# Kernel optimization log

Hardware: AMD Instinct MI355X
Metric: run time of the kernel (lower is better)

The kernel has to match this reference:

```python
import jax, jax.numpy as jnp
import numpy as np
from jax import lax

B, C, H, W = 1, 128, 56, 56
NH, NG, KS = 4, 1, 3
CG = C // NG          # channels per group
CH = C // NH          # channels per head
NHG = NH // NG        # heads per group
SCALE = CH ** -0.5


def _norm_grid(h, w, n):
    # matches _get_normalized_grid: (y, x) order, each normalized to [-1, 1]
    y = jnp.arange(h, dtype=jnp.float32) / (h - 1.0) * 2.0 - 1.0
    x = jnp.arange(w, dtype=jnp.float32) / (w - 1.0) * 2.0 - 1.0
    g = jnp.stack(jnp.meshgrid(y, x, indexing='ij'), axis=-1)  # (h, w, 2)
    return jnp.broadcast_to(g[None], (n, h, w, 2))


def _grid_sample(img, grid):
    # F.grid_sample: bilinear, align_corners=True, zeros padding; grid is (x, y) in [-1, 1]
    n, c, hi, wi = img.shape
    gs = grid.shape[1:-1]
    gx = grid[..., 0].reshape(n, -1)
    gy = grid[..., 1].reshape(n, -1)
    fx = (gx + 1.0) * 0.5 * (wi - 1)
    fy = (gy + 1.0) * 0.5 * (hi - 1)
    x0 = jnp.floor(fx)
    y0 = jnp.floor(fy)
    wx = fx - x0
    wy = fy - y0
    x0 = x0.astype(jnp.int32)
    y0 = y0.astype(jnp.int32)
    imgf = img.reshape(n, c, hi * wi)

    def corner(xi, yi, wgt):
        valid = (xi >= 0) & (xi < wi) & (yi >= 0) & (yi < hi)
        idx = jnp.clip(yi, 0, hi - 1) * wi + jnp.clip(xi, 0, wi - 1)
        vals = jax.vmap(lambda im, ii: jnp.take(im, ii, axis=1))(imgf, idx)  # (n, c, P)
        return vals * (wgt * valid)[:, None, :]

    out = (corner(x0, y0, (1 - wx) * (1 - wy)) + corner(x0 + 1, y0, wx * (1 - wy))
           + corner(x0, y0 + 1, (1 - wx) * wy) + corner(x0 + 1, y0 + 1, wx * wy))
    return out.reshape((n, c) + gs)


def _conv1x1(t, w, b):
    return jnp.einsum('bchw,oc->bohw', t, w) + b[None, :, None, None]


def _forward(x, query, dw_w, dw_b, ln_w, ln_b, pw_w, k_w, k_b, v_w, v_b, out_w, out_b, rpe_table):
    # conv_offset: depthwise 3x3 (stride 1, pad 1) -> channel LayerNorm -> GELU -> 1x1 to 2ch (no bias)
    qg = query.reshape(B * NG, CG, H, W)
    t = lax.conv_general_dilated(qg, dw_w, (1, 1), ((1, 1), (1, 1)),
                                 dimension_numbers=('NCHW', 'OIHW', 'NCHW'),
                                 feature_group_count=CG) + dw_b[None, :, None, None]
    mu = t.mean(axis=1, keepdims=True)
    var = ((t - mu) ** 2).mean(axis=1, keepdims=True)
    t = (t - mu) / jnp.sqrt(var + 1e-5) * ln_w[None, :, None, None] + ln_b[None, :, None, None]
    t = jax.nn.gelu(t, approximate=False)
    offset = jnp.einsum('bchw,oc->bohw', t, pw_w)  # (BG, 2, Hk, Wk) in (y, x) order
    Hk, Wk = offset.shape[-2:]
    n_sample = Hk * Wk

    # tanh-scaled offsets (scale_offset_range=True, factor 0.5)
    rng = jnp.array([1.0 / (Hk - 1.0), 1.0 / (Wk - 1.0)], jnp.float32).reshape(1, 2, 1, 1)
    offset = jnp.tanh(offset) * rng * 0.5
    offset = jnp.transpose(offset, (0, 2, 3, 1))  # (BG, Hk, Wk, 2)

    ref = _norm_grid(Hk, Wk, B * NG)
    rwo = offset + ref  # no clamp in the scale_offset_range branch

    # sample K/V features at deformed locations
    xs = _grid_sample(x.reshape(B * NG, CG, H, W), rwo[..., ::-1])  # (BG, CG, Hk, Wk)
    xs = xs.reshape(B, C, 1, n_sample)

    q = query.reshape(B * NH, CH, H * W)
    k = _conv1x1(xs, k_w, k_b).reshape(B * NH, CH, n_sample)
    v = _conv1x1(xs, v_w, v_b).reshape(B * NH, CH, n_sample)

    attn = jnp.einsum('bcm,bcn->bmn', q, k) * SCALE  # (B*NH, HW, n_sample)

    # relative position bias via bilinear lookup of rpe_table at displacements
    rpe = jnp.broadcast_to(rpe_table[None], (B,) + rpe_table.shape).reshape(B * NG, NHG, 2 * H - 1, 2 * W - 1)
    qgrid = _norm_grid(H, W, B * NG)
    disp = (qgrid.reshape(B * NG, H * W, 2)[:, :, None, :]
            - rwo.reshape(B * NG, n_sample, 2)[:, None, :, :]) * 0.5  # (BG, HW, n_sample, 2)
    bias = _grid_sample(rpe, disp[..., ::-1]).reshape(B * NH, H * W, n_sample)

    attn = jax.nn.softmax(attn + bias, axis=2)
    out = jnp.einsum('bmn,bcn->bcm', attn, v).reshape(B, C, H, W)
    return _conv1x1(out, out_w, out_b)


def setup_inputs() -> dict:
    key = jax.random.key(0)
    ks = jax.random.split(key, 8)
    f = lambda k, sh, s=0.02: jax.random.normal(k, sh, jnp.float32) * s
    return {
        'x': jax.random.normal(ks[0], (B, C, H, W), jnp.float32),
        'query': jax.random.normal(ks[1], (B, C, H, W), jnp.float32),
        'dw_w': f(ks[2], (CG, 1, KS, KS)),
        'dw_b': jnp.zeros((CG,), jnp.float32),
        'ln_w': jnp.ones((CG,), jnp.float32),
        'ln_b': jnp.zeros((CG,), jnp.float32),
        'pw_w': f(ks[3], (2, CG)),
        'k_w': f(ks[4], (C, C)),
        'k_b': jnp.zeros((C,), jnp.float32),
        'v_w': f(ks[5], (C, C)),
        'v_b': jnp.zeros((C,), jnp.float32),
        'out_w': f(ks[6], (C, C)),
        'out_b': jnp.zeros((C,), jnp.float32),
        'rpe_table': f(ks[7], (NH, 2 * H - 1, 2 * W - 1), 0.01),
    }


def reference(x, query, dw_w, dw_b, ln_w, ln_b, pw_w, k_w, k_b, v_w, v_b, out_w, out_b, rpe_table):
    return _forward(x, query, dw_w, dw_b, ln_w, ln_b, pw_w, k_w, k_b, v_w, v_b, out_w, out_b, rpe_table)
```

## Files before the change

kernel.cpp:

```cpp
#include <hip/hip_runtime.h>
#include <hip/hip_bf16.h>
#include <math.h>

#define HH 56
#define WW 56
#define HW 3136
#define NHEAD 4
#define RP 111
#define TP 113
#define TPE 12769
#define SCALE 0.17677669529663687f
#define LOG2E 1.44269504088896f
#define QSC (SCALE * LOG2E)
#define GHW 12544
#define NCHUNK 14
#define CLEN 224
#define BLEN 448
#define NSTEP 7

typedef unsigned short ushortT;
typedef __attribute__((ext_vector_type(8))) short short8v;
typedef __attribute__((ext_vector_type(16))) float f32x16;

#define OFF_RWO  0u
#define OFF_AA   8192u
#define OFF_W4   12288u
#define OFF_KBF  24832u
#define OFF_VBF  225536u
#define OFF_QBF  426240u
#define OFF_KWT  1028352u
#define OFF_VWT  1044736u
#define OFF_OWT  1061120u
#define OFF_XT   1077504u
#define OFF_QT   1478912u
#define OFF_TP2  1880320u
#define OFF_ATT2 1982976u
#define OFF_SUM  2384384u

__device__ __forceinline__ ushortT f2bf(float f) {
    unsigned u = __float_as_uint(f);
    u += 0x7fffu + ((u >> 16) & 1u);
    return (ushortT)(u >> 16);
}

__device__ __forceinline__ unsigned cvtpk(float lo, float hi) {
    unsigned r;
    asm("v_cvt_pk_bf16_f32 %0, %1, %2" : "=v"(r) : "v"(lo), "v"(hi));
    return r;
}

__device__ __forceinline__ float fexp2(float x) {
    float r;
    asm("v_exp_f32 %0, %1" : "=v"(r) : "v"(x));
    return r;
}

__global__ __launch_bounds__(256) void prep_all_kernel(
    const float* __restrict__ kw, const float* __restrict__ vw, const float* __restrict__ ow,
    const float* __restrict__ rpe, const float* __restrict__ x, const float* __restrict__ query,
    float* __restrict__ kwT, float* __restrict__ vwT, float* __restrict__ owT,
    float2* __restrict__ tp2, float* __restrict__ xT, float* __restrict__ qT,
    ushortT* __restrict__ qbf) {
    const int job = blockIdx.y;
    __shared__ float tile[32][33];
    if (job < 3) {
        int i = blockIdx.x * 256 + threadIdx.x;
        if (i >= 16384) return;
        const float* srcw = (job == 0) ? kw : (job == 1) ? vw : ow;
        float* dstw       = (job == 0) ? kwT : (job == 1) ? vwT : owT;
        dstw[(i & 127) * 128 + (i >> 7)] = srcw[i];
    } else if (job == 3) {
        int i = blockIdx.x * 256 + threadIdx.x;
        if (i >= NHEAD * TPE) return;
        int hd = i / TPE, r = i % TPE;
        int py = r / TP, px = r % TP;
        float v0 = 0.f, v1 = 0.f;
        if (py >= 1 && py <= RP) {
            if (px >= 1 && px <= RP) v0 = rpe[hd * RP * RP + (py - 1) * RP + (px - 1)] * LOG2E;
            if (px <= RP - 1)        v1 = rpe[hd * RP * RP + (py - 1) * RP + px] * LOG2E;
        }
        tp2[i] = make_float2(v0, v1);
    } else {
        int bx = blockIdx.x;
        if (bx >= 392) return;
        const float* src = (job == 5) ? query : x;
        float* dst       = (job == 5) ? qT : xT;
        int pt = (bx % 98) * 32, ct = (bx / 98) * 32;
        int jj = threadIdx.x & 31, ii = threadIdx.x >> 5;
#pragma unroll
        for (int r = 0; r < 4; r++)
            tile[ii + r * 8][jj] = src[(ct + ii + r * 8) * HW + pt + jj];
        __syncthreads();
#pragma unroll
        for (int r = 0; r < 4; r++) {
            int p = pt + ii + r * 8, cc = ct + jj;
            float val = tile[jj][ii + r * 8];
            dst[p * 128 + cc] = val;
            if (job == 5)
                qbf[(size_t)((cc >> 5) * HW + p) * 32 + (cc & 31)] = f2bf(val * QSC);
        }
    }
}

__device__ __forceinline__ float wave_sum(float v) {
#pragma unroll
    for (int o = 1; o < 64; o <<= 1) v += __shfl_xor(v, o);
    return v;
}

__global__ __launch_bounds__(128) void offset_kernel(
    const float* __restrict__ qT, const float* __restrict__ dww, const float* __restrict__ dwb,
    const float* __restrict__ lnw, const float* __restrict__ lnb, const float* __restrict__ pww,
    float* __restrict__ rwo, int* __restrict__ aa, float* __restrict__ w4) {
    int p = blockIdx.x;
    int c = threadIdx.x;
    int h = p / WW, w = p % WW;

    float t = dwb[c];
#pragma unroll
    for (int ky = 0; ky < 3; ky++) {
        int yy = h + ky - 1;
        if ((unsigned)yy < (unsigned)HH) {
#pragma unroll
            for (int kx = 0; kx < 3; kx++) {
                int xx = w + kx - 1;
                if ((unsigned)xx < (unsigned)WW)
                    t += qT[(yy * WW + xx) * 128 + c] * dww[c * 9 + ky * 3 + kx];
            }
        }
    }

    __shared__ float sred[4];
    int wid = c >> 6, lane0 = ((c & 63) == 0);

    float s = wave_sum(t);
    if (lane0) sred[wid] = s;
    __syncthreads();
    float mu = (sred[0] + sred[1]) * (1.f / 128.f);
    float d = t - mu;
    __syncthreads();
    s = wave_sum(d * d);
    if (lane0) sred[wid] = s;
    __syncthreads();
    float var = (sred[0] + sred[1]) * (1.f / 128.f);

    float tn = d / sqrtf(var + 1e-5f) * lnw[c] + lnb[c];
    float g = 0.5f * tn * (1.f + erff(tn * 0.70710678118654752f));

    float sy = wave_sum(g * pww[c]);
    float sx = wave_sum(g * pww[128 + c]);
    __syncthreads();
    if (lane0) { sred[wid] = sy; sred[2 + wid] = sx; }
    __syncthreads();
    if (c == 0) {
        float thy = tanhf(sred[0] + sred[1]);
        float thx = tanhf(sred[2] + sred[3]);
        rwo[p * 2]     = thy * (0.5f / 55.f) + ((float)h * (2.f / 55.f) - 1.f);
        rwo[p * 2 + 1] = thx * (0.5f / 55.f) + ((float)w * (2.f / 55.f) - 1.f);
        float ty = 55.f - (float)h - 0.25f * thy;
        float tx = 55.f - (float)w - 0.25f * thx;
        float tyf = floorf(ty), txf = floorf(tx);
        float wy = ty - tyf, wx = tx - txf;
        aa[p] = ((int)tyf) * TP + (int)txf + TP + 1;
        float4 wv;
        wv.x = (1.f - wx) * (1.f - wy);
        wv.y = wx * (1.f - wy);
        wv.z = (1.f - wx) * wy;
        wv.w = wx * wy;
        ((float4*)w4)[p] = wv;
    }
}

__global__ __launch_bounds__(128) void sample_kv_kernel(
    const float* __restrict__ xT, const float* __restrict__ rwo,
    const float* __restrict__ kwT, const float* __restrict__ vwT,
    const float* __restrict__ kb, const float* __restrict__ vb,
    ushortT* __restrict__ kbf, ushortT* __restrict__ vbf) {
    int n0 = blockIdx.x * 8;
    int tid = threadIdx.x;

    __shared__ float xs[128 * 9];
    __shared__ int   cidx[8][4];
    __shared__ float cw[8][4];
    __shared__ ushortT kst[8][128];

    if (tid < 8) {
        int n = n0 + tid;
        float gy = rwo[2 * n], gx = rwo[2 * n + 1];
        float fx = (gx + 1.f) * 27.5f;
        float fy = (gy + 1.f) * 27.5f;
        float x0f = floorf(fx), y0f = floorf(fy);
        float wx = fx - x0f, wy = fy - y0f;
        int x0 = (int)x0f, y0 = (int)y0f;
#pragma unroll
        for (int k = 0; k < 4; k++) {
            int xi = x0 + (k & 1), yi = y0 + (k >> 1);
            float wgt = ((k & 1) ? wx : 1.f - wx) * ((k >> 1) ? wy : 1.f - wy);
            bool v = (xi >= 0) && (xi < WW) && (yi >= 0) && (yi < HH);
            cidx[tid][k] = min(max(yi, 0), HH - 1) * WW + min(max(xi, 0), WW - 1);
            cw[tid][k] = v ? wgt : 0.f;
        }
    }
    __syncthreads();

#pragma unroll
    for (int j = 0; j < 8; j++) {
        float s = cw[j][0] * xT[cidx[j][0] * 128 + tid]
                + cw[j][1] * xT[cidx[j][1] * 128 + tid]
                + cw[j][2] * xT[cidx[j][2] * 128 + tid]
                + cw[j][3] * xT[cidx[j][3] * 128 + tid];
        xs[tid * 9 + j] = s;
    }
    __syncthreads();

    float ak[8], av[8];
#pragma unroll
    for (int j = 0; j < 8; j++) { ak[j] = 0.f; av[j] = 0.f; }
    for (int c = 0; c < 128; c++) {
        float wk = kwT[c * 128 + tid];
        float wv = vwT[c * 128 + tid];
#pragma unroll
        for (int j = 0; j < 8; j++) {
            float xv = xs[c * 9 + j];
            ak[j] += wk * xv;
            av[j] += wv * xv;
        }
    }
    float kbv = kb[tid], vbv = vb[tid];
    int hh = tid >> 5, ch = tid & 31;

    unsigned vp[4];
#pragma unroll
    for (int q = 0; q < 4; q++)
        vp[q] = (unsigned)f2bf(av[2 * q] + vbv) | ((unsigned)f2bf(av[2 * q + 1] + vbv) << 16);
    *(uint4*)(vbf + (size_t)(hh * 32 + ch) * HW + n0) = make_uint4(vp[0], vp[1], vp[2], vp[3]);

#pragma unroll
    for (int j = 0; j < 8; j++) kst[j][tid] = f2bf(ak[j] + kbv);
    __syncthreads();
#pragma unroll
    for (int r = 0; r < 4; r++) {
        int lin = tid + 128 * r;
        int j = lin >> 6, dd = lin & 63;
        int o = 2 * dd;
        unsigned val = *(unsigned*)&kst[j][o];
        int hd2 = o >> 5, ch2 = o & 31;
        ((unsigned*)kbf)[((size_t)(hd2 * HW + n0 + j) * 32 + ch2) >> 1] = val;
    }
}

__device__ __forceinline__ void mkw(float pa0, float pa1, float pb0, float pb1, int h,
                                    unsigned &wlo, unsigned &whi) {
    float ta0 = __shfl_xor(pa0, 32);
    float ta1 = __shfl_xor(pa1, 32);
    float tb0 = __shfl_xor(pb0, 32);
    float tb1 = __shfl_xor(pb1, 32);
    wlo = cvtpk(h ? tb0 : pa0, h ? tb1 : pa1);
    whi = cvtpk(h ? pb0 : ta0, h ? pb1 : ta1);
}

__global__ __launch_bounds__(256) void attn_kernel(
    const ushortT* __restrict__ qbf, const ushortT* __restrict__ kbf,
    const ushortT* __restrict__ vbf,
    const int* __restrict__ aa, const float4* __restrict__ w4,
    const float2* __restrict__ tp2g, float* __restrict__ att2, float* __restrict__ sums) {
    const int bx = blockIdx.x;
    const int mtile = blockIdx.y;
    const int hd = blockIdx.z;
    const int tid = threadIdx.x;
    const int wv = tid >> 6;
    const int msub = wv & 1;
    const int csub = wv >> 1;
    const int l = tid & 63;
    const int lm = l & 31;
    const int h = l >> 5;

    const int N0 = bx * BLEN;
    const int m0 = mtile * 64;
    const int mg = m0 + msub * 32 + lm;

    __shared__ int aa_s[BLEN];
    __shared__ float4 w4_s[BLEN];
    __shared__ float2 tpw[12 * TP];

    const int h_min = N0 / WW;
    const int rm0 = m0 / WW, rm1 = (m0 + 63) / WW;
    const int R0 = 48 - h_min + rm0;
    const int NR = 10 + rm1 - rm0;
    const int rbase = R0 * TP;

    const float2* srcw = tp2g + hd * TPE + rbase;
    for (int i = tid; i < NR * TP; i += 256) tpw[i] = srcw[i];
    for (int i = tid; i < BLEN; i += 256) {
        aa_s[i] = aa[N0 + i] - rbase;
        w4_s[i] = w4[N0 + i];
    }
    __syncthreads();

    const int base_m = (mg / WW) * TP + (mg % WW);

    const ushortT* qb = qbf + (size_t)(hd * HW + mg) * 32 + h * 8;
    short8v qf0 = *(const short8v*)(qb);
    short8v qf1 = *(const short8v*)(qb + 16);

    const int nwave = N0 + csub * CLEN;
    const ushortT* kbp = kbf + (size_t)(hd * HW + nwave) * 32;
    const ushortT* vbp = vbf + (size_t)(hd * 32 + lm) * HW + nwave;

    f32x16 accO;
#pragma unroll
    for (int i = 0; i < 16; i++) accO[i] = 0.f;
    float ssum = 0.f;

    for (int nt = 0; nt < NSTEP; ++nt) {
        const ushortT* ka = kbp + (size_t)(nt * 32 + lm) * 32 + h * 8;
        short8v kf0 = *(const short8v*)(ka);
        short8v kf1 = *(const short8v*)(ka + 16);
        f32x16 s;
#pragma unroll
        for (int i = 0; i < 16; i++) s[i] = 0.f;
        s = __builtin_amdgcn_mfma_f32_32x32x16_bf16(kf0, qf0, s, 0, 0, 0);
        s = __builtin_amdgcn_mfma_f32_32x32x16_bf16(kf1, qf1, s, 0, 0, 0);

        float p[16];
#pragma unroll
        for (int r = 0; r < 16; ++r) {
            int nl = csub * CLEN + nt * 32 + (r & 3) + 8 * (r >> 2) + 4 * h;
            int a0 = aa_s[nl] + base_m;
            float4 wvv = w4_s[nl];
            float2 t01 = tpw[a0];
            float2 t23 = tpw[a0 + TP];
            float bias = wvv.x * t01.x + wvv.y * t01.y + wvv.z * t23.x + wvv.w * t23.y;
            float pr = fexp2(s[r] + bias);
            ssum += pr;
            p[r] = pr;
        }

        union { unsigned u[4]; short8v s8; } A0, A1;
        mkw(p[0], p[1], p[4], p[5], h, A0.u[0], A0.u[2]);
        mkw(p[2], p[3], p[6], p[7], h, A0.u[1], A0.u[3]);
        mkw(p[8], p[9], p[12], p[13], h, A1.u[0], A1.u[2]);
        mkw(p[10], p[11], p[14], p[15], h, A1.u[1], A1.u[3]);

        const ushortT* va = vbp + nt * 32 + h * 8;
        short8v vf0 = *(const short8v*)(va);
        short8v vf1 = *(const short8v*)(va + 16);
        accO = __builtin_amdgcn_mfma_f32_32x32x16_bf16(A0.s8, vf0, accO, 0, 0, 0);
        accO = __builtin_amdgcn_mfma_f32_32x32x16_bf16(A1.s8, vf1, accO, 0, 0, 0);
    }

    float* abase = att2 + (size_t)(hd * HW + m0 + msub * 32) * 32 + lm;
#pragma unroll
    for (int r = 0; r < 16; ++r) {
        int mr = (r & 3) + 8 * (r >> 2) + 4 * h;
        atomicAdd(abase + (size_t)mr * 32, accO[r]);
    }
    float st = ssum + __shfl_xor(ssum, 32);
    if (h == 0) atomicAdd(&sums[hd * HW + mg], st);
}

__global__ __launch_bounds__(128) void combine_out_kernel(
    const float* __restrict__ att2, const float* __restrict__ sums,
    const float* __restrict__ owT, const float* __restrict__ ob, float* __restrict__ out) {
    int m0 = blockIdx.x * 8;
    int tid = threadIdx.x;
    int hd = tid >> 5, c = tid & 31;

    __shared__ float at[128 * 9];
    __shared__ float inv_s[4][8];

    if (tid < 32) {
        int hh = tid >> 3, j = tid & 7;
        inv_s[hh][j] = 1.f / sums[hh * HW + m0 + j];
    }
    __syncthreads();

#pragma unroll
    for (int j = 0; j < 8; j++)
        at[tid * 9 + j] = att2[(size_t)(hd * HW + m0 + j) * 32 + c] * inv_s[hd][j];
    __syncthreads();

    float acc[8];
#pragma unroll
    for (int j = 0; j < 8; j++) acc[j] = 0.f;
    for (int cc = 0; cc < 128; cc++) {
        float w = owT[cc * 128 + tid];
#pragma unroll
        for (int j = 0; j < 8; j++) acc[j] += w * at[cc * 9 + j];
    }
    float b = ob[tid];
#pragma unroll
    for (int j = 0; j < 8; j++) out[tid * HW + m0 + j] = acc[j] + b;
}

extern "C" void kernel_launch(void* const* d_in, const int* in_sizes, int n_in,
                              void* d_out, int out_size, void* d_ws, size_t ws_size,
                              hipStream_t stream) {
    const float* x     = (const float*)d_in[0];
    const float* query = (const float*)d_in[1];
    const float* dww   = (const float*)d_in[2];
    const float* dwb   = (const float*)d_in[3];
    const float* lnw   = (const float*)d_in[4];
    const float* lnb   = (const float*)d_in[5];
    const float* pww   = (const float*)d_in[6];
    const float* kw    = (const float*)d_in[7];
    const float* kb    = (const float*)d_in[8];
    const float* vw    = (const float*)d_in[9];
    const float* vb    = (const float*)d_in[10];
    const float* ow    = (const float*)d_in[11];
    const float* ob    = (const float*)d_in[12];
    const float* rpe   = (const float*)d_in[13];
    float* out = (float*)d_out;
    float* ws  = (float*)d_ws;

    prep_all_kernel<<<dim3(392, 6), 256, 0, stream>>>(
        kw, vw, ow, rpe, x, query,
        ws + OFF_KWT, ws + OFF_VWT, ws + OFF_OWT, (float2*)(ws + OFF_TP2),
        ws + OFF_XT, ws + OFF_QT, (ushortT*)(ws + OFF_QBF));
    offset_kernel<<<HW, 128, 0, stream>>>(ws + OFF_QT, dww, dwb, lnw, lnb, pww,
                                          ws + OFF_RWO, (int*)(ws + OFF_AA), ws + OFF_W4);
    sample_kv_kernel<<<392, 128, 0, stream>>>(ws + OFF_XT, ws + OFF_RWO,
                                              ws + OFF_KWT, ws + OFF_VWT, kb, vb,
                                              (ushortT*)(ws + OFF_KBF), (ushortT*)(ws + OFF_VBF));
    hipMemsetAsync(ws + OFF_ATT2, 0, (size_t)(401408 + 12544) * 4, stream);
    attn_kernel<<<dim3(7, 49, NHEAD), 256, 0, stream>>>(
        (const ushortT*)(ws + OFF_QBF), (const ushortT*)(ws + OFF_KBF),
        (const ushortT*)(ws + OFF_VBF),
        (const int*)(ws + OFF_AA), (const float4*)(ws + OFF_W4),
        (const float2*)(ws + OFF_TP2), ws + OFF_ATT2, ws + OFF_SUM);
    combine_out_kernel<<<392, 128, 0, stream>>>(ws + OFF_ATT2, ws + OFF_SUM,
                                                ws + OFF_OWT, ob, out);
}
```

Baseline: 162.5 us.

## Fuse offset net into sampling, memset into prep, output projection into attention tail

```diff
diff --git a/kernel.cpp b/kernel.cpp
--- a/kernel.cpp
+++ b/kernel.cpp
@@ -12,8 +12,6 @@
 #define SCALE 0.17677669529663687f
 #define LOG2E 1.44269504088896f
 #define QSC (SCALE * LOG2E)
-#define GHW 12544
-#define NCHUNK 14
 #define CLEN 224
 #define BLEN 448
 #define NSTEP 7
@@ -22,7 +20,6 @@
 typedef __attribute__((ext_vector_type(8))) short short8v;
 typedef __attribute__((ext_vector_type(16))) float f32x16;
 
-#define OFF_RWO  0u
 #define OFF_AA   8192u
 #define OFF_W4   12288u
 #define OFF_KBF  24832u
@@ -35,7 +32,9 @@
 #define OFF_QT   1478912u
 #define OFF_TP2  1880320u
 #define OFF_ATT2 1982976u
-#define OFF_SUM  2384384u
+#define OFF_SUM  (OFF_ATT2 + 401408u)
+#define OFF_CNT  (OFF_SUM + 12544u)
+#define ZERO_F4  103504u
 
 __device__ __forceinline__ ushortT f2bf(float f) {
     unsigned u = __float_as_uint(f);
@@ -53,6 +52,12 @@
     float r;
     asm("v_exp_f32 %0, %1" : "=v"(r) : "v"(x));
     return r;
+}
+
+__device__ __forceinline__ float wave_sum(float v) {
+#pragma unroll
+    for (int o = 1; o < 64; o <<= 1) v += __shfl_xor(v, o);
+    return v;
 }
 
 __global__ __launch_bounds__(256) void prep_all_kernel(
@@ -60,7 +65,7 @@
     const float* __restrict__ rpe, const float* __restrict__ x, const float* __restrict__ query,
     float* __restrict__ kwT, float* __restrict__ vwT, float* __restrict__ owT,
     float2* __restrict__ tp2, float* __restrict__ xT, float* __restrict__ qT,
-    ushortT* __restrict__ qbf) {
+    ushortT* __restrict__ qbf, float* __restrict__ zbase) {
     const int job = blockIdx.y;
     __shared__ float tile[32][33];
     if (job < 3) {
@@ -80,6 +85,9 @@
             if (px <= RP - 1)        v1 = rpe[hd * RP * RP + (py - 1) * RP + px] * LOG2E;
         }
         tp2[i] = make_float2(v0, v1);
+    } else if (job == 6) {
+        int i = blockIdx.x * 256 + threadIdx.x;
+        if (i < ZERO_F4) ((float4*)zbase)[i] = make_float4(0.f, 0.f, 0.f, 0.f);
     } else {
         int bx = blockIdx.x;
         if (bx >= 392) return;
@@ -102,91 +110,84 @@
     }
 }
 
-__device__ __forceinline__ float wave_sum(float v) {
-#pragma unroll
-    for (int o = 1; o < 64; o <<= 1) v += __shfl_xor(v, o);
-    return v;
-}
-
-__global__ __launch_bounds__(128) void offset_kernel(
-    const float* __restrict__ qT, const float* __restrict__ dww, const float* __restrict__ dwb,
-    const float* __restrict__ lnw, const float* __restrict__ lnb, const float* __restrict__ pww,
-    float* __restrict__ rwo, int* __restrict__ aa, float* __restrict__ w4) {
-    int p = blockIdx.x;
-    int c = threadIdx.x;
-    int h = p / WW, w = p % WW;
-
-    float t = dwb[c];
-#pragma unroll
-    for (int ky = 0; ky < 3; ky++) {
-        int yy = h + ky - 1;
-        if ((unsigned)yy < (unsigned)HH) {
-#pragma unroll
-            for (int kx = 0; kx < 3; kx++) {
-                int xx = w + kx - 1;
-                if ((unsigned)xx < (unsigned)WW)
-                    t += qT[(yy * WW + xx) * 128 + c] * dww[c * 9 + ky * 3 + kx];
-            }
-        }
-    }
-
-    __shared__ float sred[4];
-    int wid = c >> 6, lane0 = ((c & 63) == 0);
-
-    float s = wave_sum(t);
-    if (lane0) sred[wid] = s;
-    __syncthreads();
-    float mu = (sred[0] + sred[1]) * (1.f / 128.f);
-    float d = t - mu;
-    __syncthreads();
-    s = wave_sum(d * d);
-    if (lane0) sred[wid] = s;
-    __syncthreads();
-    float var = (sred[0] + sred[1]) * (1.f / 128.f);
-
-    float tn = d / sqrtf(var + 1e-5f) * lnw[c] + lnb[c];
-    float g = 0.5f * tn * (1.f + erff(tn * 0.70710678118654752f));
-
-    float sy = wave_sum(g * pww[c]);
-    float sx = wave_sum(g * pww[128 + c]);
-    __syncthreads();
-    if (lane0) { sred[wid] = sy; sred[2 + wid] = sx; }
-    __syncthreads();
-    if (c == 0) {
-        float thy = tanhf(sred[0] + sred[1]);
-        float thx = tanhf(sred[2] + sred[3]);
-        rwo[p * 2]     = thy * (0.5f / 55.f) + ((float)h * (2.f / 55.f) - 1.f);
-        rwo[p * 2 + 1] = thx * (0.5f / 55.f) + ((float)w * (2.f / 55.f) - 1.f);
-        float ty = 55.f - (float)h - 0.25f * thy;
-        float tx = 55.f - (float)w - 0.25f * thx;
-        float tyf = floorf(ty), txf = floorf(tx);
-        float wy = ty - tyf, wx = tx - txf;
-        aa[p] = ((int)tyf) * TP + (int)txf + TP + 1;
-        float4 wv;
-        wv.x = (1.f - wx) * (1.f - wy);
-        wv.y = wx * (1.f - wy);
-        wv.z = (1.f - wx) * wy;
-        wv.w = wx * wy;
-        ((float4*)w4)[p] = wv;
-    }
-}
-
 __global__ __launch_bounds__(128) void sample_kv_kernel(
-    const float* __restrict__ xT, const float* __restrict__ rwo,
+    const float* __restrict__ xT, const float* __restrict__ qT,
+    const float* __restrict__ dww, const float* __restrict__ dwb,
+    const float* __restrict__ lnw, const float* __restrict__ lnb,
+    const float* __restrict__ pww,
     const float* __restrict__ kwT, const float* __restrict__ vwT,
     const float* __restrict__ kb, const float* __restrict__ vb,
-    ushortT* __restrict__ kbf, ushortT* __restrict__ vbf) {
-    int n0 = blockIdx.x * 8;
-    int tid = threadIdx.x;
+    ushortT* __restrict__ kbf, ushortT* __restrict__ vbf,
+    int* __restrict__ aa, float4* __restrict__ w4g) {
+    const int n0 = blockIdx.x * 8;
+    const int tid = threadIdx.x;
+    const int h = n0 / WW, w0 = n0 % WW;
+    const int wid = tid >> 6;
+    const bool l0 = ((tid & 63) == 0);
 
     __shared__ float xs[128 * 9];
     __shared__ int   cidx[8][4];
     __shared__ float cw[8][4];
     __shared__ ushortT kst[8][128];
+    __shared__ float red_a[2][8], red_b[2][8], red_y[2][8], red_x[2][8];
+
+    float dwwr[9];
+#pragma unroll
+    for (int k = 0; k < 9; k++) dwwr[k] = dww[tid * 9 + k];
+    float qv[3][10];
+#pragma unroll
+    for (int ky = 0; ky < 3; ky++) {
+        int yy = h + ky - 1;
+        bool vy = (unsigned)yy < (unsigned)HH;
+#pragma unroll
+        for (int t = 0; t < 10; t++) {
+            int xx = w0 + t - 1;
+            bool v = vy && ((unsigned)xx < (unsigned)WW);
+            qv[ky][t] = v ? qT[(yy * WW + xx) * 128 + tid] : 0.f;
+        }
+    }
+    float tj[8];
+#pragma unroll
+    for (int j = 0; j < 8; j++) {
+        float t = dwb[tid];
+#pragma unroll
+        for (int ky = 0; ky < 3; ky++)
+#pragma unroll
+            for (int kx = 0; kx < 3; kx++)
+                t += qv[ky][j + kx] * dwwr[ky * 3 + kx];
+        tj[j] = t;
+    }
+#pragma unroll
+    for (int j = 0; j < 8; j++) { float s = wave_sum(tj[j]); if (l0) red_a[wid][j] = s; }
+    __syncthreads();
+    float dj[8];
+#pragma unroll
+    for (int j = 0; j < 8; j++) {
+        float mu = (red_a[0][j] + red_a[1][j]) * (1.f / 128.f);
+        dj[j] = tj[j] - mu;
+        float s = wave_sum(dj[j] * dj[j]);
+        if (l0) red_b[wid][j] = s;
+    }
+    __syncthreads();
+    float py = pww[tid], px = pww[128 + tid];
+#pragma unroll
+    for (int j = 0; j < 8; j++) {
+        float var = (red_b[0][j] + red_b[1][j]) * (1.f / 128.f);
+        float tn = dj[j] / sqrtf(var + 1e-5f) * lnw[tid] + lnb[tid];
+        float g = 0.5f * tn * (1.f + erff(tn * 0.70710678118654752f));
+        float sy = wave_sum(g * py);
+        float sx = wave_sum(g * px);
+        if (l0) { red_y[wid][j] = sy; red_x[wid][j] = sx; }
+    }
+    __syncthreads();
 
     if (tid < 8) {
-        int n = n0 + tid;
-        float gy = rwo[2 * n], gx = rwo[2 * n + 1];
+        int j = tid;
+        float thy = tanhf(red_y[0][j] + red_y[1][j]);
+        float thx = tanhf(red_x[0][j] + red_x[1][j]);
+        int hh = h, ww2 = w0 + j;
+        float gy = thy * (0.5f / 55.f) + ((float)hh * (2.f / 55.f) - 1.f);
+        float gx = thx * (0.5f / 55.f) + ((float)ww2 * (2.f / 55.f) - 1.f);
         float fx = (gx + 1.f) * 27.5f;
         float fy = (gy + 1.f) * 27.5f;
         float x0f = floorf(fx), y0f = floorf(fy);
@@ -197,9 +198,20 @@
             int xi = x0 + (k & 1), yi = y0 + (k >> 1);
             float wgt = ((k & 1) ? wx : 1.f - wx) * ((k >> 1) ? wy : 1.f - wy);
             bool v = (xi >= 0) && (xi < WW) && (yi >= 0) && (yi < HH);
-            cidx[tid][k] = min(max(yi, 0), HH - 1) * WW + min(max(xi, 0), WW - 1);
-            cw[tid][k] = v ? wgt : 0.f;
-        }
+            cidx[j][k] = min(max(yi, 0), HH - 1) * WW + min(max(xi, 0), WW - 1);
+            cw[j][k] = v ? wgt : 0.f;
+        }
+        float ty = 55.f - (float)hh - 0.25f * thy;
+        float tx = 55.f - (float)ww2 - 0.25f * thx;
+        float tyf = floorf(ty), txf = floorf(tx);
+        float wyb = ty - tyf, wxb = tx - txf;
+        aa[n0 + j] = ((int)tyf) * TP + (int)txf + TP + 1;
+        float4 wv;
+        wv.x = (1.f - wxb) * (1.f - wyb);
+        wv.y = wxb * (1.f - wyb);
+        wv.z = (1.f - wxb) * wyb;
+        wv.w = wxb * wyb;
+        w4g[n0 + j] = wv;
     }
     __syncthreads();
 
@@ -227,13 +239,13 @@
         }
     }
     float kbv = kb[tid], vbv = vb[tid];
-    int hh = tid >> 5, ch = tid & 31;
+    int hh2 = tid >> 5, ch = tid & 31;
 
     unsigned vp[4];
 #pragma unroll
     for (int q = 0; q < 4; q++)
         vp[q] = (unsigned)f2bf(av[2 * q] + vbv) | ((unsigned)f2bf(av[2 * q + 1] + vbv) << 16);
-    *(uint4*)(vbf + (size_t)(hh * 32 + ch) * HW + n0) = make_uint4(vp[0], vp[1], vp[2], vp[3]);
+    *(uint4*)(vbf + (size_t)(hh2 * 32 + ch) * HW + n0) = make_uint4(vp[0], vp[1], vp[2], vp[3]);
 
 #pragma unroll
     for (int j = 0; j < 8; j++) kst[j][tid] = f2bf(ak[j] + kbv);
@@ -263,7 +275,9 @@
     const ushortT* __restrict__ qbf, const ushortT* __restrict__ kbf,
     const ushortT* __restrict__ vbf,
     const int* __restrict__ aa, const float4* __restrict__ w4,
-    const float2* __restrict__ tp2g, float* __restrict__ att2, float* __restrict__ sums) {
+    const float2* __restrict__ tp2g, float* __restrict__ att2, float* __restrict__ sums,
+    int* __restrict__ cnt, const float* __restrict__ owT, const float* __restrict__ ob,
+    float* __restrict__ out) {
     const int bx = blockIdx.x;
     const int mtile = blockIdx.y;
     const int hd = blockIdx.z;
@@ -282,6 +296,8 @@
     __shared__ int aa_s[BLEN];
     __shared__ float4 w4_s[BLEN];
     __shared__ float2 tpw[12 * TP];
+    __shared__ float inv2[2][4][8];
+    __shared__ int isLast;
 
     const int h_min = N0 / WW;
     const int rm0 = m0 / WW, rm1 = (m0 + 63) / WW;
@@ -357,40 +373,43 @@
     }
     float st = ssum + __shfl_xor(ssum, 32);
     if (h == 0) atomicAdd(&sums[hd * HW + mg], st);
-}
-
-__global__ __launch_bounds__(128) void combine_out_kernel(
-    const float* __restrict__ att2, const float* __restrict__ sums,
-    const float* __restrict__ owT, const float* __restrict__ ob, float* __restrict__ out) {
-    int m0 = blockIdx.x * 8;
-    int tid = threadIdx.x;
-    int hd = tid >> 5, c = tid & 31;
-
-    __shared__ float at[128 * 9];
-    __shared__ float inv_s[4][8];
-
-    if (tid < 32) {
-        int hh = tid >> 3, j = tid & 7;
-        inv_s[hh][j] = 1.f / sums[hh * HW + m0 + j];
-    }
-    __syncthreads();
-
-#pragma unroll
-    for (int j = 0; j < 8; j++)
-        at[tid * 9 + j] = att2[(size_t)(hd * HW + m0 + j) * 32 + c] * inv_s[hd][j];
-    __syncthreads();
-
-    float acc[8];
-#pragma unroll
-    for (int j = 0; j < 8; j++) acc[j] = 0.f;
-    for (int cc = 0; cc < 128; cc++) {
-        float w = owT[cc * 128 + tid];
-#pragma unroll
-        for (int j = 0; j < 8; j++) acc[j] += w * at[cc * 9 + j];
-    }
-    float b = ob[tid];
-#pragma unroll
-    for (int j = 0; j < 8; j++) out[tid * HW + m0 + j] = acc[j] + b;
+
+    __threadfence();
+    if (tid == 0) isLast = (atomicAdd(cnt + mtile, 1) == 27) ? 1 : 0;
+    __syncthreads();
+    if (!isLast) return;
+    __threadfence();
+
+    float* atb = ((float*)tpw) + (tid >> 7) * 1184;
+    const int team = tid >> 7;
+    const int ttid = tid & 127;
+    const int hd2 = ttid >> 5, c2 = ttid & 31;
+    const float bo = ob[ttid];
+#pragma unroll 1
+    for (int it = 0; it < 4; ++it) {
+        const int r0 = m0 + team * 32 + it * 8;
+        if (ttid < 32) {
+            int hh = ttid >> 3, j = ttid & 7;
+            inv2[team][hh][j] = 1.f / sums[hh * HW + r0 + j];
+        }
+        __syncthreads();
+#pragma unroll
+        for (int j = 0; j < 8; ++j)
+            atb[ttid * 9 + j] = att2[(size_t)(hd2 * HW + r0 + j) * 32 + c2] * inv2[team][hd2][j];
+        __syncthreads();
+        float acc[8];
+#pragma unroll
+        for (int j = 0; j < 8; ++j) acc[j] = 0.f;
+        for (int cc = 0; cc < 128; ++cc) {
+            float wgt = owT[cc * 128 + ttid];
+            const float* arow = atb + cc * 9;
+#pragma unroll
+            for (int j = 0; j < 8; ++j) acc[j] += wgt * arow[j];
+        }
+#pragma unroll
+        for (int j = 0; j < 8; ++j) out[ttid * HW + r0 + j] = acc[j] + bo;
+        __syncthreads();
+    }
 }
 
 extern "C" void kernel_launch(void* const* d_in, const int* in_sizes, int n_in,
@@ -413,21 +432,19 @@
     float* out = (float*)d_out;
     float* ws  = (float*)d_ws;
 
-    prep_all_kernel<<<dim3(392, 6), 256, 0, stream>>>(
+    prep_all_kernel<<<dim3(405, 7), 256, 0, stream>>>(
         kw, vw, ow, rpe, x, query,
         ws + OFF_KWT, ws + OFF_VWT, ws + OFF_OWT, (float2*)(ws + OFF_TP2),
-        ws + OFF_XT, ws + OFF_QT, (ushortT*)(ws + OFF_QBF));
-    offset_kernel<<<HW, 128, 0, stream>>>(ws + OFF_QT, dww, dwb, lnw, lnb, pww,
-                                          ws + OFF_RWO, (int*)(ws + OFF_AA), ws + OFF_W4);
-    sample_kv_kernel<<<392, 128, 0, stream>>>(ws + OFF_XT, ws + OFF_RWO,
-                                              ws + OFF_KWT, ws + OFF_VWT, kb, vb,
-                                              (ushortT*)(ws + OFF_KBF), (ushortT*)(ws + OFF_VBF));
-    hipMemsetAsync(ws + OFF_ATT2, 0, (size_t)(401408 + 12544) * 4, stream);
+        ws + OFF_XT, ws + OFF_QT, (ushortT*)(ws + OFF_QBF), ws + OFF_ATT2);
+    sample_kv_kernel<<<392, 128, 0, stream>>>(
+        ws + OFF_XT, ws + OFF_QT, dww, dwb, lnw, lnb, pww,
+        ws + OFF_KWT, ws + OFF_VWT, kb, vb,
+        (ushortT*)(ws + OFF_KBF), (ushortT*)(ws + OFF_VBF),
+        (int*)(ws + OFF_AA), (float4*)(ws + OFF_W4));
     attn_kernel<<<dim3(7, 49, NHEAD), 256, 0, stream>>>(
         (const ushortT*)(ws + OFF_QBF), (const ushortT*)(ws + OFF_KBF),
         (const ushortT*)(ws + OFF_VBF),
         (const int*)(ws + OFF_AA), (const float4*)(ws + OFF_W4),
-        (const float2*)(ws + OFF_TP2), ws + OFF_ATT2, ws + OFF_SUM);
-    combine_out_kernel<<<392, 128, 0, stream>>>(ws + OFF_ATT2, ws + OFF_SUM,
-                                                ws + OFF_OWT, ob, out);
-}
+        (const float2*)(ws + OFF_TP2), ws + OFF_ATT2, ws + OFF_SUM,
+        (int*)(ws + OFF_CNT), ws + OFF_OWT, ob, out);
+}
```

Result: slower. 267.2 us (+64.5%).
